# Kernel optimization log

Measured on AMD Instinct MI355X. Metric: run time of the kernel, lower is better.

Reference implementation:

```python
import jax, jax.numpy as jnp
import numpy as np

NUM_GROUPS1 = 8
NUM_GROUPS2 = 4
NUM_HEADS = 8


def setup_inputs() -> dict:
    key = jax.random.key(0)
    k1, k2, k3 = jax.random.split(key, 3)
    B, N, C = 8, 4096, 512
    x = jax.random.normal(k1, (B, N, C), dtype=jnp.float32)
    # torch Linear(dim, 3*inner_dim, bias=False); stored transposed for x @ W
    W_qkv = jax.random.normal(k2, (C, 3 * C), dtype=jnp.float32) * 0.02
    W_proj = jax.random.normal(k3, (C, C), dtype=jnp.float32) * 0.02
    b_proj = jnp.zeros((C,), dtype=jnp.float32)
    return {"x": x, "W_qkv": W_qkv, "W_proj": W_proj, "b_proj": b_proj,
            "recursive_index": 0}


def reference(x, W_qkv, W_proj, b_proj, recursive_index):
    # recursive_index is a static Python int (0 -> False branch, num_groups1).
    num_groups = NUM_GROUPS1 if not recursive_index else NUM_GROUPS2
    B, N, C = x.shape
    H = NUM_HEADS
    Dh = C // H
    scale = Dh ** -0.5
    Np = int(np.ceil(N / num_groups) * num_groups)
    if Np != N:
        x = jnp.pad(x, ((0, 0), (0, Np - N), (0, 0)))
    L = Np // num_groups  # tokens per group
    # qkv projection, then split into per-group per-head tensors [B,G,H,L,Dh]
    qkv = (x @ W_qkv).reshape(B, num_groups, L, 3, H, Dh)
    q = jnp.transpose(qkv[:, :, :, 0], (0, 1, 3, 2, 4))
    k = jnp.transpose(qkv[:, :, :, 1], (0, 1, 3, 2, 4))
    v = jnp.transpose(qkv[:, :, :, 2], (0, 1, 3, 2, 4))
    attn = jax.nn.softmax(jnp.einsum('bghld,bghmd->bghlm', q, k) * scale, axis=-1)
    out = jnp.einsum('bghlm,bghmd->bghld', attn, v)  # [B,G,H,L,Dh]
    out = jnp.transpose(out, (0, 1, 3, 2, 4)).reshape(B, Np, C)[:, :N]
    return out @ W_proj + b_proj
```

## Files before the change

### kernel.cpp

```cpp
#include <hip/hip_runtime.h>
#include <hip/hip_bf16.h>

typedef __attribute__((ext_vector_type(8))) short  bf16x8;
typedef __attribute__((ext_vector_type(4))) float  f32x4;

__device__ __forceinline__ ushort f2bf(float f) {
    unsigned u = __builtin_bit_cast(unsigned, f);
    u += 0x7fffu + ((u >> 16) & 1u);
    return (ushort)(u >> 16);
}

__device__ __forceinline__ unsigned cvt_pk_bf16(float a, float b) {
    unsigned r;
    asm("v_cvt_pk_bf16_f32 %0, %1, %2" : "=v"(r) : "v"(a), "v"(b));
    return r;
}

__device__ __forceinline__ void gload_lds16(const ushort* g, ushort* l) {
    __builtin_amdgcn_global_load_lds(
        (const __attribute__((address_space(1))) void*)(g),
        (__attribute__((address_space(3))) void*)(l), 16, 0, 0);
}

__device__ __forceinline__ void blockbar() {
    asm volatile("" ::: "memory");
    __builtin_amdgcn_sched_barrier(0);
    __builtin_amdgcn_s_barrier();
    __builtin_amdgcn_sched_barrier(0);
    asm volatile("" ::: "memory");
}
#define SFENCE() __builtin_amdgcn_sched_barrier(0)

__global__ __launch_bounds__(256) void prep_kernel(
        const float* __restrict__ x, ushort* __restrict__ xb,
        const float* __restrict__ Wqkv, ushort* __restrict__ wq,
        const float* __restrict__ Wproj, ushort* __restrict__ wp) {
    __shared__ ushort t[64 * 65];
    const int bx = blockIdx.x, tid = threadIdx.x;
    if (bx < 16384) {
        int i = bx * 256 + tid;
        float4 f = reinterpret_cast<const float4*>(x)[i];
        ushort4 o;
        o.x = f2bf(f.x); o.y = f2bf(f.y); o.z = f2bf(f.z); o.w = f2bf(f.w);
        reinterpret_cast<ushort4*>(xb)[i] = o;
        return;
    }
    const float* in; ushort* out; int Cc, qcols, cB, rB; float qs;
    if (bx < 16576) {
        int b2 = bx - 16384;
        in = Wqkv; out = wq; Cc = 1536; qcols = 512;
        qs = 0.18033688011112043f;
        cB = (b2 % 24) * 64; rB = (b2 / 24) * 64;
    } else {
        int b2 = bx - 16576;
        in = Wproj; out = wp; Cc = 512; qcols = 0; qs = 1.0f;
        cB = (b2 % 8) * 64; rB = (b2 / 8) * 64;
    }
#pragma unroll
    for (int p = 0; p < 16; ++p) {
        int lin = p * 256 + tid;
        int r = lin >> 6, c = lin & 63;
        float v = in[(size_t)(rB + r) * Cc + cB + c];
        if (cB + c < qcols) v *= qs;
        t[c * 65 + r] = f2bf(v);
    }
    __syncthreads();
#pragma unroll
    for (int p = 0; p < 16; ++p) {
        int lin = p * 256 + tid;
        int c = lin >> 6, r = lin & 63;
        out[(size_t)(cB + c) * 512 + rB + r] = t[c * 65 + r];
    }
}

template<bool F32OUT, bool SPLIT_VT>
__global__ __launch_bounds__(512, 2) void gemm_bt_kernel(
        const ushort* __restrict__ A, const ushort* __restrict__ Bt,
        void* __restrict__ Cout, const float* __restrict__ bias,
        const ushort* __restrict__ Wv, ushort* __restrict__ vT,
        int Ncols, int K) {
    __shared__ ushort smem[65536];
    const int tid = threadIdx.x;
    const int id  = blockIdx.x;
    const bool vt = SPLIT_VT && (id >= 512);
    const ushort* Amat; const ushort* Bmat; int mBase, nBase;
    if (!vt) {
        Amat = A; Bmat = Bt;
        mBase = ((id & 7) * 16 + ((id >> 3) & 15)) << 8;
        nBase = (id >> 7) << 8;
    } else {
        int vid = id - 512;
        Amat = Wv; Bmat = A;
        mBase = (vid >> 7) << 8;
        nBase = ((vid & 7) * 16 + ((vid >> 3) & 15)) << 8;
    }
    const int w = tid >> 6, lane = tid & 63, ml = lane & 15, quad = lane >> 4;
    const int wr = (w >> 2) * 128, wc = (w & 3) * 64;

    const int srow = lane >> 3;
    const int sch  = (lane & 7) ^ srow;
    const ushort* Ap = Amat + (size_t)(mBase + w * 32 + srow) * K + sch * 8;
    const ushort* Bp = Bmat + (size_t)(nBase + w * 32 + srow) * K + sch * 8;

    f32x4 z4 = {0.f, 0.f, 0.f, 0.f};
    f32x4 acc[8][4];
#pragma unroll
    for (int i = 0; i < 8; ++i)
#pragma unroll
        for (int j = 0; j < 4; ++j) acc[i][j] = z4;

    auto stage = [&](int t, int slot) {
        ushort* la_ = smem + slot * 32768;
        ushort* lb_ = la_ + 16384;
        const ushort* a = Ap + t * 64;
        const ushort* b = Bp + t * 64;
#pragma unroll
        for (int i = 0; i < 4; ++i) {
            gload_lds16(a + (size_t)(8 * i) * K, la_ + (w * 32 + 8 * i) * 64);
            gload_lds16(b + (size_t)(8 * i) * K, lb_ + (w * 32 + 8 * i) * 64);
        }
    };

    const int rdo0 = ((0 + quad) ^ (ml & 7)) << 3;
    const int rdo1 = ((4 + quad) ^ (ml & 7)) << 3;

    auto compute = [&](int slot) {
        ushort* la_ = smem + slot * 32768;
        ushort* lb_ = la_ + 16384;
        bf16x8 bv[4][2];
#pragma unroll
        for (int fn = 0; fn < 4; ++fn) {
            ushort* r = lb_ + (wc + fn * 16 + ml) * 64;
            bv[fn][0] = *reinterpret_cast<bf16x8*>(r + rdo0);
            bv[fn][1] = *reinterpret_cast<bf16x8*>(r + rdo1);
        }
#pragma unroll
        for (int mh = 0; mh < 2; ++mh) {
            bf16x8 af[4][2];
#pragma unroll
            for (int fm = 0; fm < 4; ++fm) {
                ushort* r = la_ + (wr + mh * 64 + fm * 16 + ml) * 64;
                af[fm][0] = *reinterpret_cast<bf16x8*>(r + rdo0);
                af[fm][1] = *reinterpret_cast<bf16x8*>(r + rdo1);
            }
            __builtin_amdgcn_s_setprio(1);
#pragma unroll
            for (int ks = 0; ks < 2; ++ks)
#pragma unroll
                for (int fm = 0; fm < 4; ++fm)
#pragma unroll
                    for (int fn = 0; fn < 4; ++fn)
                        acc[mh * 4 + fm][fn] = __builtin_amdgcn_mfma_f32_16x16x32_bf16(
                            af[fm][ks], bv[fn][ks], acc[mh * 4 + fm][fn], 0, 0, 0);
            __builtin_amdgcn_s_setprio(0);
        }
    };

    const int nkt = K >> 6;
    stage(0, 0); SFENCE();
    stage(1, 1); SFENCE();
    for (int t = 0; t < nkt - 1; ++t) {
        asm volatile("s_waitcnt vmcnt(8)" ::: "memory");
        blockbar();
        compute(t & 1);
        blockbar();
        if (t + 2 < nkt) { stage(t + 2, t & 1); SFENCE(); }
    }
    asm volatile("s_waitcnt vmcnt(0)" ::: "memory");
    blockbar();
    compute((nkt - 1) & 1);

    if (F32OUT) {
        float* ep = reinterpret_cast<float*>(smem) + w * 1088;
        float bj[4];
#pragma unroll
        for (int j = 0; j < 4; ++j) bj[j] = bias[nBase + wc + j * 16 + ml];
        float* cbase = reinterpret_cast<float*>(Cout);
#pragma unroll
        for (int i = 0; i < 8; ++i) {
#pragma unroll
            for (int j = 0; j < 4; ++j)
#pragma unroll
                for (int r = 0; r < 4; ++r)
                    ep[(quad * 4 + r) * 68 + j * 16 + ml] = acc[i][j][r] + bj[j];
#pragma unroll
            for (int t = 0; t < 4; ++t) {
                int ch = quad + 4 * t;
                float4 v = *reinterpret_cast<const float4*>(ep + ml * 68 + ch * 4);
                *reinterpret_cast<float4*>(cbase
                    + (size_t)(mBase + wr + i * 16 + ml) * Ncols + nBase + wc + ch * 4) = v;
            }
        }
    } else {
        ushort* ep = smem + w * 1152;
#pragma unroll
        for (int i = 0; i < 8; ++i) {
#pragma unroll
            for (int j = 0; j < 4; ++j)
#pragma unroll
                for (int r = 0; r < 4; ++r)
                    ep[(quad * 4 + r) * 72 + j * 16 + ml] = f2bf(acc[i][j][r]);
#pragma unroll
            for (int t = 0; t < 2; ++t) {
                int ch = quad + 4 * t;
                bf16x8 v = *reinterpret_cast<const bf16x8*>(ep + ml * 72 + ch * 8);
                int row = mBase + wr + i * 16 + ml;
                if (!vt) {
                    *reinterpret_cast<bf16x8*>(reinterpret_cast<ushort*>(Cout)
                        + (size_t)row * Ncols + nBase + wc + ch * 8) = v;
                } else {
                    *reinterpret_cast<bf16x8*>(vT
                        + ((size_t)((nBase >> 9) * 512 + row)) * 512
                        + (nBase & 511) + wc + ch * 8) = v;
                }
            }
        }
    }
}

__global__ __launch_bounds__(256) void attn_kernel(
        const ushort* __restrict__ qk, const ushort* __restrict__ vT,
        ushort* __restrict__ out) {
    __shared__ ushort k_lds[64 * 64];
    __shared__ ushort v_lds[64 * 64];
    __shared__ ushort p_lds[4 * 32 * 72];
    const int tid = threadIdx.x;
    const int w = tid >> 6, lane = tid & 63, ml = lane & 15, quad = lane >> 4;
    const int id = blockIdx.x;
    const int bgh = id >> 2, qc = id & 3;
    const int b = bgh >> 6, g = (bgh >> 3) & 7, h = bgh & 7;
    const int tb = b * 4096 + g * 512;
    const ushort* base  = qk + (size_t)tb * 1024 + h * 64;
    const ushort* vbase = vT + ((size_t)((b * 8 + g) * 512 + h * 64)) * 512;
    const int qOff = qc * 128 + w * 32;

    bf16x8 qf[2][2];
#pragma unroll
    for (int qb = 0; qb < 2; ++qb)
#pragma unroll
        for (int ks = 0; ks < 2; ++ks)
            qf[qb][ks] = *reinterpret_cast<const bf16x8*>(
                base + (size_t)(qOff + qb * 16 + ml) * 1024 + ks * 32 + quad * 8);

    const int srow = lane >> 3;
    const int sch  = (lane & 7) ^ srow;
    const ushort* kp = base + (size_t)(w * 16 + srow) * 1024 + 512 + sch * 8;
    ushort* kdst = k_lds + (w * 16) * 64;
    const ushort* vp = vbase + (size_t)(w * 16 + srow) * 512 + sch * 8;
    ushort* vdst = v_lds + (w * 16) * 64;

    const bf16x8 onesf = {0x3f80, 0x3f80, 0x3f80, 0x3f80,
                          0x3f80, 0x3f80, 0x3f80, 0x3f80};

    f32x4 z4 = {0.f, 0.f, 0.f, 0.f};
    f32x4 oacc[2][4];
    f32x4 sacc[2];
#pragma unroll
    for (int qb = 0; qb < 2; ++qb) {
#pragma unroll
        for (int db = 0; db < 4; ++db) oacc[qb][db] = z4;
        sacc[qb] = z4;
    }

    ushort* pw = p_lds + w * 32 * 72;
    for (int kt = 0; kt < 8; ++kt) {
        gload_lds16(kp + (size_t)(kt * 64) * 1024,     kdst);
        gload_lds16(kp + (size_t)(kt * 64 + 8) * 1024, kdst + 8 * 64);
        gload_lds16(vp + kt * 64,           vdst);
        gload_lds16(vp + 8 * 512 + kt * 64, vdst + 8 * 64);
        __syncthreads();

        f32x4 s[2][4];
#pragma unroll
        for (int qb = 0; qb < 2; ++qb)
#pragma unroll
            for (int kb = 0; kb < 4; ++kb) s[qb][kb] = z4;
#pragma unroll
        for (int ks = 0; ks < 2; ++ks) {
            bf16x8 kfs[4];
#pragma unroll
            for (int kb = 0; kb < 4; ++kb)
                kfs[kb] = *reinterpret_cast<bf16x8*>(
                    k_lds + (kb * 16 + ml) * 64 + (((ks * 4 + quad) ^ (ml & 7)) << 3));
#pragma unroll
            for (int qb = 0; qb < 2; ++qb)
#pragma unroll
                for (int kb = 0; kb < 4; ++kb)
                    s[qb][kb] = __builtin_amdgcn_mfma_f32_16x16x32_bf16(kfs[kb], qf[qb][ks], s[qb][kb], 0, 0, 0);
        }

#pragma unroll
        for (int qb = 0; qb < 2; ++qb)
#pragma unroll
            for (int kb = 0; kb < 4; ++kb) {
                float p0 = exp2f(s[qb][kb][0]), p1 = exp2f(s[qb][kb][1]);
                float p2 = exp2f(s[qb][kb][2]), p3 = exp2f(s[qb][kb][3]);
                uint2 pk2;
                pk2.x = cvt_pk_bf16(p0, p1);
                pk2.y = cvt_pk_bf16(p2, p3);
                *reinterpret_cast<uint2*>(
                    pw + (qb * 16 + ml) * 72 + kb * 16 + quad * 4) = pk2;
            }

#pragma unroll
        for (int ks = 0; ks < 2; ++ks) {
            bf16x8 pfs[2], vfs[4];
#pragma unroll
            for (int qb = 0; qb < 2; ++qb)
                pfs[qb] = *reinterpret_cast<bf16x8*>(
                    pw + (qb * 16 + ml) * 72 + ks * 32 + quad * 8);
#pragma unroll
            for (int db = 0; db < 4; ++db)
                vfs[db] = *reinterpret_cast<bf16x8*>(
                    v_lds + (db * 16 + ml) * 64 + (((ks * 4 + quad) ^ (ml & 7)) << 3));
#pragma unroll
            for (int qb = 0; qb < 2; ++qb)
                sacc[qb] = __builtin_amdgcn_mfma_f32_16x16x32_bf16(pfs[qb], onesf, sacc[qb], 0, 0, 0);
#pragma unroll
            for (int qb = 0; qb < 2; ++qb)
#pragma unroll
                for (int db = 0; db < 4; ++db)
                    oacc[qb][db] = __builtin_amdgcn_mfma_f32_16x16x32_bf16(pfs[qb], vfs[db], oacc[qb][db], 0, 0, 0);
        }
        __syncthreads();
    }

    float invq[2][4];
#pragma unroll
    for (int qb = 0; qb < 2; ++qb)
#pragma unroll
        for (int r = 0; r < 4; ++r)
            invq[qb][r] = 1.0f / sacc[qb][r];
#pragma unroll
    for (int qb = 0; qb < 2; ++qb)
#pragma unroll
        for (int db = 0; db < 4; ++db)
#pragma unroll
            for (int r = 0; r < 4; ++r) {
                float v = oacc[qb][db][r] * invq[qb][r];
                out[(size_t)(tb + qOff + qb * 16 + quad * 4 + r) * 512
                    + h * 64 + db * 16 + ml] = f2bf(v);
            }
}

extern "C" void kernel_launch(void* const* d_in, const int* in_sizes, int n_in,
                              void* d_out, int out_size, void* d_ws, size_t ws_size,
                              hipStream_t stream) {
    const float* x     = (const float*)d_in[0];
    const float* Wqkv  = (const float*)d_in[1];
    const float* Wproj = (const float*)d_in[2];
    const float* bproj = (const float*)d_in[3];

    char* ws = (char*)d_ws;
    ushort* xb   = (ushort*)(ws);
    ushort* wq   = (ushort*)(ws + 33554432);
    ushort* wp   = (ushort*)(ws + 35127296);
    ushort* qkb  = (ushort*)(ws + 35651584);
    ushort* vTb  = (ushort*)(ws + 102760448);
    ushort* attn = xb;
    ushort* wv   = wq + 1024 * 512;
    float*  outp = (float*)d_out;

    prep_kernel<<<16640, 256, 0, stream>>>(x, xb, Wqkv, wq, Wproj, wp);
    gemm_bt_kernel<false, true><<<768, 512, 0, stream>>>(
        xb, wq, qkb, nullptr, wv, vTb, 1024, 512);
    attn_kernel<<<2048, 256, 0, stream>>>(qkb, vTb, attn);
    gemm_bt_kernel<true, false><<<256, 512, 0, stream>>>(
        attn, wp, outp, bproj, nullptr, nullptr, 512, 512);
}
```

Before: 279.9 us.

## Double-buffer K/V LDS tiles in attention kernel and reorder block mapping

The attention kernel now uses two LDS buffers for the K and V tiles, issuing global-to-LDS loads two tiles ahead and waiting with explicit vmcnt counts, so loads overlap MFMA compute. The block index mapping is changed so query chunks of the same (b,g,h) land in different launch waves, and s_setprio is raised around the MFMA bursts. The cost is twice the LDS for K/V, which may reduce occupancy, and the correctness of the pipeline depends on the hand-written vmcnt values.

After: 282.6 us. Within noise of the previous version (+0.9%).

```diff
diff --git a/kernel.cpp b/kernel.cpp
--- a/kernel.cpp
+++ b/kernel.cpp
@@ -221,13 +221,13 @@
 __global__ __launch_bounds__(256) void attn_kernel(
         const ushort* __restrict__ qk, const ushort* __restrict__ vT,
         ushort* __restrict__ out) {
-    __shared__ ushort k_lds[64 * 64];
-    __shared__ ushort v_lds[64 * 64];
+    __shared__ ushort k_lds[2][64 * 64];
+    __shared__ ushort v_lds[2][64 * 64];
     __shared__ ushort p_lds[4 * 32 * 72];
     const int tid = threadIdx.x;
     const int w = tid >> 6, lane = tid & 63, ml = lane & 15, quad = lane >> 4;
     const int id = blockIdx.x;
-    const int bgh = id >> 2, qc = id & 3;
+    const int bgh = id & 511, qc = id >> 9;
     const int b = bgh >> 6, g = (bgh >> 3) & 7, h = bgh & 7;
     const int tb = b * 4096 + g * 512;
     const ushort* base  = qk + (size_t)tb * 1024 + h * 64;
@@ -241,13 +241,19 @@
         for (int ks = 0; ks < 2; ++ks)
             qf[qb][ks] = *reinterpret_cast<const bf16x8*>(
                 base + (size_t)(qOff + qb * 16 + ml) * 1024 + ks * 32 + quad * 8);
+    SFENCE();
 
     const int srow = lane >> 3;
     const int sch  = (lane & 7) ^ srow;
     const ushort* kp = base + (size_t)(w * 16 + srow) * 1024 + 512 + sch * 8;
-    ushort* kdst = k_lds + (w * 16) * 64;
     const ushort* vp = vbase + (size_t)(w * 16 + srow) * 512 + sch * 8;
-    ushort* vdst = v_lds + (w * 16) * 64;
+
+    auto stage = [&](int kt, int buf) {
+        gload_lds16(kp + (size_t)(kt * 64) * 1024,     k_lds[buf] + (w * 16) * 64);
+        gload_lds16(kp + (size_t)(kt * 64 + 8) * 1024, k_lds[buf] + (w * 16 + 8) * 64);
+        gload_lds16(vp + kt * 64,           v_lds[buf] + (w * 16) * 64);
+        gload_lds16(vp + 8 * 512 + kt * 64, v_lds[buf] + (w * 16 + 8) * 64);
+    };
 
     const bf16x8 onesf = {0x3f80, 0x3f80, 0x3f80, 0x3f80,
                           0x3f80, 0x3f80, 0x3f80, 0x3f80};
@@ -263,13 +269,8 @@
     }
 
     ushort* pw = p_lds + w * 32 * 72;
-    for (int kt = 0; kt < 8; ++kt) {
-        gload_lds16(kp + (size_t)(kt * 64) * 1024,     kdst);
-        gload_lds16(kp + (size_t)(kt * 64 + 8) * 1024, kdst + 8 * 64);
-        gload_lds16(vp + kt * 64,           vdst);
-        gload_lds16(vp + 8 * 512 + kt * 64, vdst + 8 * 64);
-        __syncthreads();
-
+
+    auto compute = [&](int buf) {
         f32x4 s[2][4];
 #pragma unroll
         for (int qb = 0; qb < 2; ++qb)
@@ -281,12 +282,14 @@
 #pragma unroll
             for (int kb = 0; kb < 4; ++kb)
                 kfs[kb] = *reinterpret_cast<bf16x8*>(
-                    k_lds + (kb * 16 + ml) * 64 + (((ks * 4 + quad) ^ (ml & 7)) << 3));
+                    k_lds[buf] + (kb * 16 + ml) * 64 + (((ks * 4 + quad) ^ (ml & 7)) << 3));
+            __builtin_amdgcn_s_setprio(1);
 #pragma unroll
             for (int qb = 0; qb < 2; ++qb)
 #pragma unroll
                 for (int kb = 0; kb < 4; ++kb)
                     s[qb][kb] = __builtin_amdgcn_mfma_f32_16x16x32_bf16(kfs[kb], qf[qb][ks], s[qb][kb], 0, 0, 0);
+            __builtin_amdgcn_s_setprio(0);
         }
 
 #pragma unroll
@@ -312,7 +315,8 @@
 #pragma unroll
             for (int db = 0; db < 4; ++db)
                 vfs[db] = *reinterpret_cast<bf16x8*>(
-                    v_lds + (db * 16 + ml) * 64 + (((ks * 4 + quad) ^ (ml & 7)) << 3));
+                    v_lds[buf] + (db * 16 + ml) * 64 + (((ks * 4 + quad) ^ (ml & 7)) << 3));
+            __builtin_amdgcn_s_setprio(1);
 #pragma unroll
             for (int qb = 0; qb < 2; ++qb)
                 sacc[qb] = __builtin_amdgcn_mfma_f32_16x16x32_bf16(pfs[qb], onesf, sacc[qb], 0, 0, 0);
@@ -321,9 +325,22 @@
 #pragma unroll
                 for (int db = 0; db < 4; ++db)
                     oacc[qb][db] = __builtin_amdgcn_mfma_f32_16x16x32_bf16(pfs[qb], vfs[db], oacc[qb][db], 0, 0, 0);
-        }
-        __syncthreads();
-    }
+            __builtin_amdgcn_s_setprio(0);
+        }
+    };
+
+    stage(0, 0); SFENCE();
+    stage(1, 1); SFENCE();
+    for (int kt = 0; kt < 7; ++kt) {
+        asm volatile("s_waitcnt vmcnt(4)" ::: "memory");
+        blockbar();
+        compute(kt & 1);
+        blockbar();
+        if (kt + 2 < 8) { stage(kt + 2, kt & 1); SFENCE(); }
+    }
+    asm volatile("s_waitcnt vmcnt(0)" ::: "memory");
+    blockbar();
+    compute(1);
 
     float invq[2][4];
 #pragma unroll
```

## Prefetch K/V tiles through registers, remap block order, raise MFMA priority

Applied to the files above, without the earlier changes.

The attention kernel now prefetches the next K/V tile into registers while the current tile is computed from LDS, then writes it to LDS after a barrier. This replaces the load-then-wait loop in which every iteration stalled on its global loads. Block indices are remapped so that consecutive blocks cover different heads of the same query chunk. MFMA sections are wrapped in s_setprio to favor matrix issue. The prefetch costs more registers and adds an LDS write stage with extra barriers per iteration.

Result: no change. 284.2 us (+1.5%).

```diff
diff --git a/kernel.cpp b/kernel.cpp
--- a/kernel.cpp
+++ b/kernel.cpp
@@ -227,7 +227,8 @@
     const int tid = threadIdx.x;
     const int w = tid >> 6, lane = tid & 63, ml = lane & 15, quad = lane >> 4;
     const int id = blockIdx.x;
-    const int bgh = id >> 2, qc = id & 3;
+    const int qc = (id >> 3) & 3;
+    const int bgh = (id & 7) | ((id >> 5) << 3);
     const int b = bgh >> 6, g = (bgh >> 3) & 7, h = bgh & 7;
     const int tb = b * 4096 + g * 512;
     const ushort* base  = qk + (size_t)tb * 1024 + h * 64;
@@ -241,13 +242,17 @@
         for (int ks = 0; ks < 2; ++ks)
             qf[qb][ks] = *reinterpret_cast<const bf16x8*>(
                 base + (size_t)(qOff + qb * 16 + ml) * 1024 + ks * 32 + quad * 8);
+    SFENCE();
 
     const int srow = lane >> 3;
     const int sch  = (lane & 7) ^ srow;
     const ushort* kp = base + (size_t)(w * 16 + srow) * 1024 + 512 + sch * 8;
-    ushort* kdst = k_lds + (w * 16) * 64;
     const ushort* vp = vbase + (size_t)(w * 16 + srow) * 512 + sch * 8;
-    ushort* vdst = v_lds + (w * 16) * 64;
+    ushort* kdst0 = k_lds + (w * 16) * 64;
+    ushort* kdst1 = k_lds + (w * 16 + 8) * 64;
+    ushort* vdst0 = v_lds + (w * 16) * 64;
+    ushort* vdst1 = v_lds + (w * 16 + 8) * 64;
+    const int wds = lane * 8;
 
     const bf16x8 onesf = {0x3f80, 0x3f80, 0x3f80, 0x3f80,
                           0x3f80, 0x3f80, 0x3f80, 0x3f80};
@@ -263,13 +268,8 @@
     }
 
     ushort* pw = p_lds + w * 32 * 72;
-    for (int kt = 0; kt < 8; ++kt) {
-        gload_lds16(kp + (size_t)(kt * 64) * 1024,     kdst);
-        gload_lds16(kp + (size_t)(kt * 64 + 8) * 1024, kdst + 8 * 64);
-        gload_lds16(vp + kt * 64,           vdst);
-        gload_lds16(vp + 8 * 512 + kt * 64, vdst + 8 * 64);
-        __syncthreads();
-
+
+    auto compute = [&]() {
         f32x4 s[2][4];
 #pragma unroll
         for (int qb = 0; qb < 2; ++qb)
@@ -282,11 +282,13 @@
             for (int kb = 0; kb < 4; ++kb)
                 kfs[kb] = *reinterpret_cast<bf16x8*>(
                     k_lds + (kb * 16 + ml) * 64 + (((ks * 4 + quad) ^ (ml & 7)) << 3));
+            __builtin_amdgcn_s_setprio(1);
 #pragma unroll
             for (int qb = 0; qb < 2; ++qb)
 #pragma unroll
                 for (int kb = 0; kb < 4; ++kb)
                     s[qb][kb] = __builtin_amdgcn_mfma_f32_16x16x32_bf16(kfs[kb], qf[qb][ks], s[qb][kb], 0, 0, 0);
+            __builtin_amdgcn_s_setprio(0);
         }
 
 #pragma unroll
@@ -313,6 +315,7 @@
             for (int db = 0; db < 4; ++db)
                 vfs[db] = *reinterpret_cast<bf16x8*>(
                     v_lds + (db * 16 + ml) * 64 + (((ks * 4 + quad) ^ (ml & 7)) << 3));
+            __builtin_amdgcn_s_setprio(1);
 #pragma unroll
             for (int qb = 0; qb < 2; ++qb)
                 sacc[qb] = __builtin_amdgcn_mfma_f32_16x16x32_bf16(pfs[qb], onesf, sacc[qb], 0, 0, 0);
@@ -321,8 +324,41 @@
 #pragma unroll
                 for (int db = 0; db < 4; ++db)
                     oacc[qb][db] = __builtin_amdgcn_mfma_f32_16x16x32_bf16(pfs[qb], vfs[db], oacc[qb][db], 0, 0, 0);
-        }
-        __syncthreads();
+            __builtin_amdgcn_s_setprio(0);
+        }
+    };
+
+    gload_lds16(kp,             kdst0);
+    gload_lds16(kp + 8 * 1024,  kdst1);
+    gload_lds16(vp,             vdst0);
+    gload_lds16(vp + 8 * 512,   vdst1);
+    SFENCE();
+    uint4 kr0 = *reinterpret_cast<const uint4*>(kp + (size_t)64 * 1024);
+    uint4 kr1 = *reinterpret_cast<const uint4*>(kp + (size_t)72 * 1024);
+    uint4 vr0 = *reinterpret_cast<const uint4*>(vp + 64);
+    uint4 vr1 = *reinterpret_cast<const uint4*>(vp + 8 * 512 + 64);
+    SFENCE();
+    asm volatile("s_waitcnt vmcnt(4)" ::: "memory");
+    blockbar();
+
+    for (int kt = 0; kt < 8; ++kt) {
+        compute();
+        if (kt < 7) {
+            asm volatile("s_waitcnt vmcnt(0)" ::: "memory");
+            __syncthreads();
+            *reinterpret_cast<uint4*>(kdst0 + wds) = kr0;
+            *reinterpret_cast<uint4*>(kdst1 + wds) = kr1;
+            *reinterpret_cast<uint4*>(vdst0 + wds) = vr0;
+            *reinterpret_cast<uint4*>(vdst1 + wds) = vr1;
+            if (kt + 2 < 8) {
+                kr0 = *reinterpret_cast<const uint4*>(kp + (size_t)((kt + 2) * 64) * 1024);
+                kr1 = *reinterpret_cast<const uint4*>(kp + (size_t)((kt + 2) * 64 + 8) * 1024);
+                vr0 = *reinterpret_cast<const uint4*>(vp + (kt + 2) * 64);
+                vr1 = *reinterpret_cast<const uint4*>(vp + 8 * 512 + (kt + 2) * 64);
+            }
+            asm volatile("s_waitcnt lgkmcnt(0)" ::: "memory");
+            blockbar();
+        }
     }
 
     float invq[2][4];
```
